# Performance work log

Measured on AMD Instinct MI355X. Metric: run time of the kernel, lower is better.

## Reference

```python
import jax, jax.numpy as jnp
import numpy as np

EPS = 1e-5
NEG_SLOPE = 0.2  # DGL GATConv default leaky_relu slope


def conv1d_same(x, w, b):
    # x: [N, Cin, T], w: [Cout, Cin, K]
    y = jax.lax.conv_general_dilated(x, w, (1,), 'SAME',
                                     dimension_numbers=('NCW', 'OIW', 'NCW'))
    return y + b[None, :, None]


def gated_conv(x, w1, b1, w2, b2, w3, b3):
    # Temporal_Gated_Conv: relu(conv1(x)*sigmoid(conv2(x)) + conv3(x))
    return jax.nn.relu(conv1d_same(x, w1, b1) * jax.nn.sigmoid(conv1d_same(x, w2, b2))
                       + conv1d_same(x, w3, b3))


def bn3(x, g, b):
    # BatchNorm1d on [N, C, T]: stats over (N, T), training mode (batch stats)
    m = jnp.mean(x, (0, 2), keepdims=True)
    v = jnp.var(x, (0, 2), keepdims=True)
    return (x - m) * jax.lax.rsqrt(v + EPS) * g[None, :, None] + b[None, :, None]


def bn2(x, g, b):
    # BatchNorm1d on [N, F]: stats over N
    m = jnp.mean(x, 0, keepdims=True)
    v = jnp.var(x, 0, keepdims=True)
    return (x - m) * jax.lax.rsqrt(v + EPS) * g[None, :] + b[None, :]


def setup_inputs() -> dict:
    key = jax.random.key(0)
    ks = jax.random.split(key, 24)
    N, C, T, H, DEG = 20000, 32, 8, 4, 16
    F = C * T          # GAT in/out feats per head = 256
    E = N * DEG
    s = 0.05
    inp = {
        'X': jax.random.normal(ks[0], (N, C, T), jnp.float32),
        'src': jax.random.randint(ks[1], (E,), 0, N, jnp.int32),
        'dst': jax.random.randint(ks[2], (E,), 0, N, jnp.int32),
        # residual_proj: Conv1d(C->C, k=1)
        'rp_w': jax.random.normal(ks[3], (C, C, 1), jnp.float32) * s,
        'rp_b': jnp.zeros((C,), jnp.float32),
        # gated_conv1: three Conv1d(C->C, k=3)
        'g1_w1': jax.random.normal(ks[4], (C, C, 3), jnp.float32) * s,
        'g1_b1': jnp.zeros((C,), jnp.float32),
        'g1_w2': jax.random.normal(ks[5], (C, C, 3), jnp.float32) * s,
        'g1_b2': jnp.zeros((C,), jnp.float32),
        'g1_w3': jax.random.normal(ks[6], (C, C, 3), jnp.float32) * s,
        'g1_b3': jnp.zeros((C,), jnp.float32),
        'bn0_g': jnp.ones((C,), jnp.float32),
        'bn0_b': jnp.zeros((C,), jnp.float32),
        # GATConv: fc [H*F, F], attn_l/attn_r [H, F], bias [H*F]
        'gat_w': jax.random.normal(ks[7], (H * F, F), jnp.float32) * s,
        'attn_l': jax.random.normal(ks[8], (H, F), jnp.float32) * s,
        'attn_r': jax.random.normal(ks[9], (H, F), jnp.float32) * s,
        'gat_bias': jnp.zeros((H * F,), jnp.float32),
        'bn1_g': jnp.ones((H * F,), jnp.float32),
        'bn1_b': jnp.zeros((H * F,), jnp.float32),
        # gated_conv2: three Conv1d(C*H -> C, k=3)
        'g2_w1': jax.random.normal(ks[10], (C, C * H, 3), jnp.float32) * s,
        'g2_b1': jnp.zeros((C,), jnp.float32),
        'g2_w2': jax.random.normal(ks[11], (C, C * H, 3), jnp.float32) * s,
        'g2_b2': jnp.zeros((C,), jnp.float32),
        'g2_w3': jax.random.normal(ks[12], (C, C * H, 3), jnp.float32) * s,
        'g2_b3': jnp.zeros((C,), jnp.float32),
        'bn2_g': jnp.ones((C,), jnp.float32),
        'bn2_b': jnp.zeros((C,), jnp.float32),
    }
    return inp


def reference(X, src, dst, rp_w, rp_b, g1_w1, g1_b1, g1_w2, g1_b2, g1_w3, g1_b3,
              bn0_g, bn0_b, gat_w, attn_l, attn_r, gat_bias, bn1_g, bn1_b,
              g2_w1, g2_b1, g2_w2, g2_b2, g2_w3, g2_b3, bn2_g, bn2_b):
    N, C, T = X.shape
    H, F = attn_l.shape

    residual = conv1d_same(X, rp_w, rp_b)                      # [N, C, T]
    x = gated_conv(X, g1_w1, g1_b1, g1_w2, g1_b2, g1_w3, g1_b3)
    x = bn3(x, bn0_g, bn0_b)
    x = x.reshape(N, C * T)                                    # row-major flatten == torch .view

    # --- DGL GATConv (feat_drop=attn_drop=0, concat heads, ReLU activation) ---
    h = (x @ gat_w.T).reshape(N, H, F)                         # fc projection
    el = jnp.sum(h * attn_l, -1)                               # [N, H]
    er = jnp.sum(h * attn_r, -1)                               # [N, H]
    e = jax.nn.leaky_relu(el[src] + er[dst], NEG_SLOPE)        # [E, H]
    # segment softmax over incoming edges of each dst node
    m = jax.ops.segment_max(e, dst, num_segments=N)            # [N, H]
    ee = jnp.exp(e - m[dst])
    den = jax.ops.segment_sum(ee, dst, num_segments=N)         # [N, H]
    alpha = ee / den[dst]                                      # [E, H]
    rst = jax.ops.segment_sum(alpha[:, :, None] * h[src], dst, num_segments=N)  # [N, H, F]
    rst = jax.nn.relu(rst + gat_bias.reshape(H, F))

    x = rst.reshape(N, H * F)                                  # concat heads
    x = bn2(x, bn1_g, bn1_b)
    x = x.reshape(N, (H * F) // T, T)                          # [N, C*H, T]
    x = gated_conv(x, g2_w1, g2_b1, g2_w2, g2_b2, g2_w3, g2_b3)
    x = bn3(x, bn2_g, bn2_b)
    x = jax.nn.relu(x + residual)                              # self.last=True, dropout=0
    return x
```

## Files before the change

kernel.cpp:

```cpp
#include <hip/hip_runtime.h>
#include <stdint.h>

#define NN 20000
#define NE 320000

typedef unsigned short us16;
typedef __attribute__((ext_vector_type(8))) short short8;
typedef __attribute__((ext_vector_type(4))) float f32x4;

union U4 { uint4 v; us16 s[8]; unsigned u[4]; };
union U2 { uint2 v; us16 s[4]; };

__device__ __forceinline__ float b2f(us16 u){ return __uint_as_float(((unsigned)u)<<16); }
__device__ __forceinline__ us16 f2b(float f){
  unsigned u = __float_as_uint(f);
  u += 0x7fffu + ((u>>16)&1u);
  return (us16)(u>>16);
}

__global__ __launch_bounds__(256) void k_misc(
    const float* __restrict__ gatw, us16* __restrict__ Wb,
    const float* __restrict__ w1, const float* __restrict__ w2, const float* __restrict__ w3,
    us16* __restrict__ Wt,
    const float* __restrict__ c1w1, const float* __restrict__ c1w2, const float* __restrict__ c1w3,
    const float* __restrict__ rp_w, us16* __restrict__ Wt1,
    const float* __restrict__ attnl, const float* __restrict__ attnr,
    float* __restrict__ wl, float* __restrict__ wr,
    const int* __restrict__ dst, int* __restrict__ counts)
{
  const int b = blockIdx.x, tid = threadIdx.x;
  if(b < 256){
    int i = b*256 + tid;
    float4 v = *(const float4*)(gatw + (size_t)i*4);
    U2 o;
    o.s[0]=f2b(v.x); o.s[1]=f2b(v.y); o.s[2]=f2b(v.z); o.s[3]=f2b(v.w);
    *(uint2*)(Wb + (size_t)i*4) = o.v;
  } else if(b < 400){
    int i = (b-256)*256 + tid;
    int s = i/12288, rem = i%12288;
    int co3 = rem>>7, ci = rem&127;
    const float* w = (co3<32) ? w1 : (co3<64) ? w2 : w3;
    Wt[i] = f2b(w[(co3&31)*384 + ci*3 + s]);
  } else if(b < 448){
    int i = (b-400)*256 + tid;
    int s = i>>12, rem = i&4095;
    int co3 = rem>>5, ci = rem&31;
    float v;
    if(co3 < 96){
      const float* w = (co3<32) ? c1w1 : (co3<64) ? c1w2 : c1w3;
      v = w[(co3&31)*96 + ci*3 + s];
    } else {
      v = (s==1) ? rp_w[(co3-96)*32 + ci] : 0.f;
    }
    Wt1[i] = f2b(v);
  } else if(b < 480){
    int bb = b-448;
    int sel = bb>>4, hd = (bb>>2)&3, fq = bb&3;
    const float* attn = sel ? attnr : attnl;
    int k = tid;
    float s = 0.f;
    int f0 = fq*64;
    #pragma unroll 8
    for(int f=f0; f<f0+64; f++)
      s = fmaf(attn[hd*256+f], gatw[(size_t)(hd*256+f)*256 + k], s);
    atomicAdd(&((sel ? wr : wl)[hd*256+k]), s);
  } else {
    int e = (b-480)*256 + tid;
    if(e < NE) atomicAdd(&counts[dst[e]], 1);
  }
}

__global__ __launch_bounds__(256) void k_gemm1(
    const float* __restrict__ X, const us16* __restrict__ Wt1,
    const float* __restrict__ b1, const float* __restrict__ b2, const float* __restrict__ b3,
    const float* __restrict__ rp_b,
    us16* __restrict__ gc1, us16* __restrict__ resid,
    float* __restrict__ bn0_sum, float* __restrict__ bn0_sq)
{
  __shared__ float smemF[16896];
  us16* As = (us16*)smemF;
  us16* Bs = As + 6400;
  float* Cs = smemF;
  __shared__ float redS[32], redQ[32];
  const int tid = threadIdx.x;
  if(tid<32){ redS[tid]=0.f; redQ[tid]=0.f; }
  const int node0 = blockIdx.x*16;
  const int lane = tid&63, wv = tid>>6;
  const int wm = wv&1, wn = wv>>1;
  const int mrow = lane&15, kg = (lane>>4)*8;
  for(int idx=tid; idx<1024; idx+=256){
    int n = idx>>6, rem = idx&63, slot = (rem>>5)*9, ci = rem&31;
    As[n*400 + slot*40 + ci] = 0;
  }
  #pragma unroll
  for(int i=0;i<4;i++){
    int idx = i*256 + tid;
    int n = idx>>6, rem = idx&63, ci = rem>>1, tq = rem&1;
    float4 xv = *(const float4*)(X + (size_t)(node0+n)*256 + ci*8 + tq*4);
    us16* p = &As[n*400 + (tq*4+1)*40 + ci];
    p[0]   = f2b(xv.x);
    p[40]  = f2b(xv.y);
    p[80]  = f2b(xv.z);
    p[120] = f2b(xv.w);
  }
  #pragma unroll
  for(int i=0;i<6;i++){
    int c = i*256 + tid;
    int s = c>>9, rem = c&511, co = rem>>2, cq = rem&3;
    *(uint4*)&Bs[s*5120 + co*40 + cq*8] = *(const uint4*)(Wt1 + s*4096 + co*32 + cq*8);
  }
  __syncthreads();
  f32x4 acc[4][4] = {};
  #pragma unroll
  for(int s=0; s<3; s++){
    short8 af[4], bfr[4];
    #pragma unroll
    for(int i=0;i<4;i++){
      int r = wm*64 + i*16 + mrow;
      af[i] = *(const short8*)&As[(r>>3)*400 + ((r&7)+s)*40 + kg];
    }
    #pragma unroll
    for(int j=0;j<4;j++)
      bfr[j] = *(const short8*)&Bs[s*5120 + (wn*64 + j*16 + mrow)*40 + kg];
    #pragma unroll
    for(int i=0;i<4;i++){
      #pragma unroll
      for(int j=0;j<4;j++)
        acc[i][j] = __builtin_amdgcn_mfma_f32_16x16x32_bf16(af[i], bfr[j], acc[i][j], 0, 0, 0);
    }
  }
  __syncthreads();
  #pragma unroll
  for(int i=0;i<4;i++){
    #pragma unroll
    for(int j=0;j<4;j++){
      #pragma unroll
      for(int r=0;r<4;r++)
        Cs[(wm*64 + i*16 + (lane>>4)*4 + r)*132 + wn*64 + j*16 + (lane&15)] = acc[i][j][r];
    }
  }
  __syncthreads();
  const int co = tid&31, rg = tid>>5;
  const float bb1=b1[co], bb2=b2[co], bb3=b3[co], bbr=rp_b[co];
  float s=0.f, q=0.f;
  #pragma unroll
  for(int half=0; half<2; half++){
    U4 ov, rv;
    #pragma unroll
    for(int t=0;t<8;t++){
      int r = rg*16 + half*8 + t;
      float c1 = Cs[r*132 + co]      + bb1;
      float c2 = Cs[r*132 + co + 32] + bb2;
      float c3 = Cs[r*132 + co + 64] + bb3;
      float rr = Cs[r*132 + co + 96] + bbr;
      float sg = 1.f/(1.f+__expf(-c2));
      float v = fmaf(c1, sg, c3);
      v = v>0.f ? v : 0.f;
      s += v; q += v*v;
      ov.s[t] = f2b(v);
      rv.s[t] = f2b(rr);
    }
    int node = node0 + rg*2 + half;
    *(uint4*)(gc1   + (size_t)node*256 + co*8) = ov.v;
    *(uint4*)(resid + (size_t)node*256 + co*8) = rv.v;
  }
  atomicAdd(&redS[co], s); atomicAdd(&redQ[co], q);
  __syncthreads();
  if(tid<32)      atomicAdd(&bn0_sum[tid], redS[tid]);
  else if(tid<64) atomicAdd(&bn0_sq[tid-32], redQ[tid-32]);
}

__global__ __launch_bounds__(256) void k_eler2(const us16* __restrict__ gc1,
    const float* __restrict__ bn0_sum, const float* __restrict__ bn0_sq,
    const float* __restrict__ bn0g, const float* __restrict__ bn0b,
    const float* __restrict__ wl, const float* __restrict__ wr,
    float* __restrict__ el, float* __restrict__ er,
    const int* __restrict__ counts, int* __restrict__ offsets, int* __restrict__ cursor)
{
  const int tid = threadIdx.x;
  if(blockIdx.x < 5000){
    __shared__ float sa[32], sb[32];
    if(tid<32){
      float m = bn0_sum[tid]*(1.f/160000.f);
      float v = bn0_sq[tid]*(1.f/160000.f) - m*m;
      float a = bn0g[tid]*rsqrtf(v + 1e-5f);
      sa[tid] = a; sb[tid] = bn0b[tid] - m*a;
    }
    __syncthreads();
    const int wv = tid>>6, lane = tid&63;
    const int node = blockIdx.x*4 + wv;
    U2 g; g.v = *(const uint2*)(gc1 + (size_t)node*256 + lane*4);
    const float a = sa[lane>>1], b = sb[lane>>1];
    float xv[4];
    #pragma unroll
    for(int j=0;j<4;j++) xv[j] = fmaf(a, b2f(g.s[j]), b);
    float res[8];
    #pragma unroll
    for(int hd=0; hd<4; hd++){
      float4 lv = *(const float4*)(wl + hd*256 + lane*4);
      float4 rv = *(const float4*)(wr + hd*256 + lane*4);
      res[hd]   = xv[0]*lv.x + xv[1]*lv.y + xv[2]*lv.z + xv[3]*lv.w;
      res[4+hd] = xv[0]*rv.x + xv[1]*rv.y + xv[2]*rv.z + xv[3]*rv.w;
    }
    #pragma unroll
    for(int o=32;o;o>>=1){
      #pragma unroll
      for(int k=0;k<8;k++) res[k] += __shfl_xor(res[k], o, 64);
    }
    if(lane==0){
      #pragma unroll
      for(int hd=0;hd<4;hd++){ el[node*4+hd]=res[hd]; er[node*4+hd]=res[4+hd]; }
    }
  } else {
    __shared__ int buf[256];
    const int base = tid*79;
    int s = 0;
    for(int j=0;j<79;j++){
      int idx = base+j;
      if(idx<NN) s += counts[idx];
    }
    buf[tid] = s;
    __syncthreads();
    for(int off=1; off<256; off<<=1){
      int t = (tid>=off) ? buf[tid-off] : 0;
      __syncthreads();
      buf[tid] += t;
      __syncthreads();
    }
    int excl = buf[tid] - s;
    for(int j=0;j<79;j++){
      int idx = base+j;
      if(idx<NN){
        offsets[idx]=excl; cursor[idx]=excl;
        excl += counts[idx];
      }
    }
    if(tid==255) offsets[NN] = buf[255];
  }
}

__global__ __launch_bounds__(256) void k_scatter(const int* __restrict__ src, const int* __restrict__ dst,
    int* __restrict__ cursor, int* __restrict__ esrc,
    const float* __restrict__ el, const float* __restrict__ er,
    float* __restrict__ ew)
{
  int e = blockIdx.x*256 + threadIdx.x;
  if(e < NE){
    int s = src[e], d = dst[e];
    int pos = atomicAdd(&cursor[d], 1);
    esrc[pos] = s;
    float4 lv = *(const float4*)(el + s*4);
    float4 rv = *(const float4*)(er + d*4);
    float4 sc;
    sc.x = lv.x+rv.x; sc.x = sc.x>0.f ? sc.x : 0.2f*sc.x;
    sc.y = lv.y+rv.y; sc.y = sc.y>0.f ? sc.y : 0.2f*sc.y;
    sc.z = lv.z+rv.z; sc.z = sc.z>0.f ? sc.z : 0.2f*sc.z;
    sc.w = lv.w+rv.w; sc.w = sc.w>0.f ? sc.w : 0.2f*sc.w;
    *(float4*)(ew + (size_t)pos*4) = sc;
  }
}

__global__ __launch_bounds__(256) void k_agg2(
    const int* __restrict__ offsets, const int* __restrict__ esrc,
    const float* __restrict__ ew, const us16* __restrict__ gc1,
    const float* __restrict__ bn0_sum, const float* __restrict__ bn0_sq,
    const float* __restrict__ bn0g, const float* __restrict__ bn0b,
    us16* __restrict__ Axg)
{
  const int tid = threadIdx.x;
  const int wv = tid>>6, lane = tid&63;
  const int node = blockIdx.x*4 + wv;
  const int ch = lane>>1;
  float mmn = bn0_sum[ch]*(1.f/160000.f);
  float vvn = bn0_sq[ch]*(1.f/160000.f) - mmn*mmn;
  float sa = bn0g[ch]*rsqrtf(vvn + 1e-5f);
  float sb = bn0b[ch] - mmn*sa;
  const int beg = offsets[node];
  const int deg = offsets[node+1] - beg;
  const int h = lane>>4, i0 = lane&15;
  float m = -3.0e38f;
  for(int i=i0; i<deg; i+=16) m = fmaxf(m, ew[(size_t)(beg+i)*4 + h]);
  m = fmaxf(m, __shfl_xor(m,1,64)); m = fmaxf(m, __shfl_xor(m,2,64));
  m = fmaxf(m, __shfl_xor(m,4,64)); m = fmaxf(m, __shfl_xor(m,8,64));
  float den = 0.f;
  for(int i=i0; i<deg; i+=16) den += __expf(ew[(size_t)(beg+i)*4 + h] - m);
  den += __shfl_xor(den,1,64); den += __shfl_xor(den,2,64);
  den += __shfl_xor(den,4,64); den += __shfl_xor(den,8,64);
  const float m0=__shfl(m,0,64),   m1=__shfl(m,16,64),  m2=__shfl(m,32,64),  m3=__shfl(m,48,64);
  const float d0=__shfl(den,0,64), d1=__shfl(den,16,64),d2=__shfl(den,32,64),d3=__shfl(den,48,64);
  const float v0=d0>0.f?1.f/d0:0.f, v1=d1>0.f?1.f/d1:0.f,
              v2=d2>0.f?1.f/d2:0.f, v3=d3>0.f?1.f/d3:0.f;
  float a0c[4]={},a1c[4]={},a2c[4]={},a3c[4]={};
  #pragma unroll 4
  for(int j=0; j<deg; j++){
    int pos = beg+j;
    float4 w4 = *(const float4*)(ew + (size_t)pos*4);
    int sN = esrc[pos];
    U2 hv; hv.v = *(const uint2*)(gc1 + (size_t)sN*256 + lane*4);
    float e0 = __expf(w4.x-m0)*v0;
    float e1 = __expf(w4.y-m1)*v1;
    float e2 = __expf(w4.z-m2)*v2;
    float e3 = __expf(w4.w-m3)*v3;
    #pragma unroll
    for(int kk=0;kk<4;kk++){
      float x = b2f(hv.s[kk]);
      a0c[kk] = fmaf(e0,x,a0c[kk]);
      a1c[kk] = fmaf(e1,x,a1c[kk]);
      a2c[kk] = fmaf(e2,x,a2c[kk]);
      a3c[kk] = fmaf(e3,x,a3c[kk]);
    }
  }
  const float sbi = sb * ((deg>0)?1.f:0.f);
  U2 o0,o1,o2,o3;
  #pragma unroll
  for(int kk=0;kk<4;kk++){
    o0.s[kk]=f2b(fmaf(sa,a0c[kk],sbi));
    o1.s[kk]=f2b(fmaf(sa,a1c[kk],sbi));
    o2.s[kk]=f2b(fmaf(sa,a2c[kk],sbi));
    o3.s[kk]=f2b(fmaf(sa,a3c[kk],sbi));
  }
  *(uint2*)(Axg + ((size_t)node)*256            + lane*4) = o0.v;
  *(uint2*)(Axg + ((size_t)NN + node)*256       + lane*4) = o1.v;
  *(uint2*)(Axg + ((size_t)2*NN + node)*256     + lane*4) = o2.v;
  *(uint2*)(Axg + ((size_t)3*NN + node)*256     + lane*4) = o3.v;
}

__global__ __launch_bounds__(256) void k_gemm3(const us16* __restrict__ Axg, const us16* __restrict__ Wb,
    const float* __restrict__ gbias, us16* __restrict__ rst,
    float* __restrict__ bn1_sum, float* __restrict__ bn1_sq)
{
  __shared__ us16 As[128*40];
  __shared__ us16 Bs[128*40];
  const int tid = threadIdx.x;
  const int row0 = blockIdx.x*128;
  const int cb   = blockIdx.y*128;
  const int hd   = blockIdx.z;
  const us16* A = Axg + (size_t)hd*NN*256;
  const us16* B = Wb  + (size_t)(hd*256 + cb)*256;
  const int lane = tid&63, wv = tid>>6;
  const int wm = wv&1, wn = wv>>1;
  const int mrow = lane&15, kg = (lane>>4)*8;
  f32x4 acc[4][4] = {};
  for(int k0=0; k0<256; k0+=32){
    #pragma unroll
    for(int i=0;i<2;i++){
      int chunk = i*256 + tid;
      int row = chunk>>2, cc = chunk&3;
      int g = row0 + row;
      uint4 av; av.x=0;av.y=0;av.z=0;av.w=0;
      if(g < NN) av = *(const uint4*)(A + (size_t)g*256 + k0 + cc*8);
      *(uint4*)&As[row*40 + cc*8] = av;
      *(uint4*)&Bs[row*40 + cc*8] = *(const uint4*)(B + (size_t)row*256 + k0 + cc*8);
    }
    __syncthreads();
    short8 af[4], bfr[4];
    #pragma unroll
    for(int i=0;i<4;i++) af[i]  = *(const short8*)&As[(wm*64 + i*16 + mrow)*40 + kg];
    #pragma unroll
    for(int j=0;j<4;j++) bfr[j] = *(const short8*)&Bs[(wn*64 + j*16 + mrow)*40 + kg];
    #pragma unroll
    for(int i=0;i<4;i++){
      #pragma unroll
      for(int j=0;j<4;j++)
        acc[i][j] = __builtin_amdgcn_mfma_f32_16x16x32_bf16(af[i], bfr[j], acc[i][j], 0, 0, 0);
    }
    __syncthreads();
  }
  float gb[4];
  #pragma unroll
  for(int j=0;j<4;j++)
    gb[j] = gbias[hd*256 + cb + wn*64 + j*16 + (lane&15)];
  float cs[4]={}, cq[4]={};
  #pragma unroll
  for(int i=0;i<4;i++){
    #pragma unroll
    for(int j=0;j<4;j++){
      #pragma unroll
      for(int r=0;r<4;r++){
        int g = row0 + wm*64 + i*16 + (lane>>4)*4 + r;
        if(g < NN){
          float v = acc[i][j][r] + gb[j];
          v = v>0.f ? v : 0.f;
          rst[(size_t)g*1024 + hd*256 + cb + wn*64 + j*16 + (lane&15)] = f2b(v);
          cs[j] += v; cq[j] += v*v;
        }
      }
    }
  }
  #pragma unroll
  for(int j=0;j<4;j++){
    cs[j] += __shfl_xor(cs[j],16,64); cs[j] += __shfl_xor(cs[j],32,64);
    cq[j] += __shfl_xor(cq[j],16,64); cq[j] += __shfl_xor(cq[j],32,64);
  }
  if(lane < 16){
    #pragma unroll
    for(int j=0;j<4;j++){
      int col = hd*256 + cb + wn*64 + j*16 + lane;
      atomicAdd(&bn1_sum[col], cs[j]);
      atomicAdd(&bn1_sq[col],  cq[j]);
    }
  }
}

__global__ __launch_bounds__(256) void k_gemm2(
    const us16* __restrict__ rst, const us16* __restrict__ Wt,
    const float* __restrict__ bn1_sum, const float* __restrict__ bn1_sq,
    const float* __restrict__ bn1g, const float* __restrict__ bn1b,
    const float* __restrict__ b1, const float* __restrict__ b2, const float* __restrict__ b3,
    us16* __restrict__ y2, float* __restrict__ bn2_sum, float* __restrict__ bn2_sq)
{
  __shared__ float smemF[16384];
  float* s1a = smemF;
  float* s1b = smemF + 1024;
  us16* As = (us16*)(smemF + 2048);
  us16* Bs = As + 21760;
  float* Cs = (float*)(smemF + 2048);
  __shared__ float redS[32], redQ[32];
  const int tid = threadIdx.x;
  if(tid<32){ redS[tid]=0.f; redQ[tid]=0.f; }
  const int node0 = blockIdx.x*16;
  const int lane = tid&63, wv = tid>>6;
  const int wm = wv&1, wn = wv>>1;
  const int mrow = lane&15, kg = (lane>>4)*8;
  for(int f=tid; f<1024; f+=256){
    float m = bn1_sum[f]*(1.f/20000.f);
    float v = bn1_sq[f]*(1.f/20000.f) - m*m;
    float a = bn1g[f]*rsqrtf(v + 1e-5f);
    int l = (f&7)*128 + (f>>3);
    s1a[l] = a; s1b[l] = bn1b[f] - m*a;
  }
  for(int idx=tid; idx<4096; idx+=256){
    int n = idx>>8, rem = idx&255, slot = (rem>>7)*9, ci = rem&127;
    As[n*1360 + slot*136 + ci] = 0;
  }
  __syncthreads();
  #pragma unroll
  for(int i=0;i<8;i++){
    int idx = i*256 + tid;
    int n = idx>>7, ci = idx&127;
    U4 in; in.v = *(const uint4*)(rst + (size_t)(node0+n)*1024 + ci*8);
    us16* p = &As[n*1360 + 136 + ci];
    #pragma unroll
    for(int t=0;t<8;t++){
      float a = s1a[t*128+ci], b = s1b[t*128+ci];
      p[t*136] = f2b(fmaf(a, b2f(in.s[t]), b));
    }
  }
  f32x4 acc[4][3] = {};
  for(int rd=0; rd<6; rd++){
    const int s = rd>>1, kc = rd&1;
    __syncthreads();
    #pragma unroll
    for(int i=0;i<3;i++){
      int chunk = i*256 + tid;
      int brow = chunk>>3, cc = chunk&7;
      *(uint4*)&Bs[brow*72 + cc*8] =
        *(const uint4*)(Wt + s*12288 + brow*128 + kc*64 + cc*8);
    }
    __syncthreads();
    #pragma unroll
    for(int kk=0; kk<64; kk+=32){
      short8 af[4], bfr[3];
      #pragma unroll
      for(int i=0;i<4;i++){
        int r = wm*64 + i*16 + mrow;
        af[i] = *(const short8*)&As[(r>>3)*1360 + ((r&7)+s)*136 + kc*64 + kk + kg];
      }
      #pragma unroll
      for(int j=0;j<3;j++)
        bfr[j] = *(const short8*)&Bs[(wn*48 + j*16 + mrow)*72 + kk + kg];
      #pragma unroll
      for(int i=0;i<4;i++){
        #pragma unroll
        for(int j=0;j<3;j++)
          acc[i][j] = __builtin_amdgcn_mfma_f32_16x16x32_bf16(af[i], bfr[j], acc[i][j], 0, 0, 0);
      }
    }
  }
  __syncthreads();
  #pragma unroll
  for(int i=0;i<4;i++){
    #pragma unroll
    for(int j=0;j<3;j++){
      #pragma unroll
      for(int r=0;r<4;r++)
        Cs[(wm*64 + i*16 + (lane>>4)*4 + r)*100 + wn*48 + j*16 + (lane&15)] = acc[i][j][r];
    }
  }
  __syncthreads();
  const int co = tid&31, rg = tid>>5;
  const float bb1=b1[co], bb2=b2[co], bb3=b3[co];
  float s=0.f, q=0.f;
  #pragma unroll
  for(int half=0; half<2; half++){
    U4 ov;
    #pragma unroll
    for(int t=0;t<8;t++){
      int r = rg*16 + half*8 + t;
      float c1 = Cs[r*100 + co]      + bb1;
      float c2 = Cs[r*100 + co + 32] + bb2;
      float c3 = Cs[r*100 + co + 64] + bb3;
      float sg = 1.f/(1.f+__expf(-c2));
      float v = fmaf(c1, sg, c3);
      v = v>0.f ? v : 0.f;
      s += v; q += v*v;
      ov.s[t] = f2b(v);
    }
    int node = node0 + rg*2 + half;
    *(uint4*)(y2 + (size_t)node*256 + co*8) = ov.v;
  }
  atomicAdd(&redS[co], s); atomicAdd(&redQ[co], q);
  __syncthreads();
  if(tid<32)      atomicAdd(&bn2_sum[tid], redS[tid]);
  else if(tid<64) atomicAdd(&bn2_sq[tid-32], redQ[tid-32]);
}

__global__ __launch_bounds__(256) void k_final(const us16* __restrict__ y2,
    const float* __restrict__ bn2_sum, const float* __restrict__ bn2_sq,
    const float* __restrict__ bn2g, const float* __restrict__ bn2b,
    const us16* __restrict__ resid, float* __restrict__ out)
{
  __shared__ float fa[32], fb[32];
  const int tid = threadIdx.x;
  if(tid<32){
    float m = bn2_sum[tid]*(1.f/160000.f);
    float v = bn2_sq[tid]*(1.f/160000.f) - m*m;
    float a = bn2g[tid]*rsqrtf(v + 1e-5f);
    fa[tid] = a; fb[tid] = bn2b[tid] - m*a;
  }
  __syncthreads();
  size_t base = ((size_t)blockIdx.x*256 + tid)*8;
  int ch = (int)((base>>3)&31);
  float a = fa[ch], b = fb[ch];
  U4 yv, rv;
  yv.v = *(const uint4*)(y2+base);
  rv.v = *(const uint4*)(resid+base);
  float4 o0, o1;
  float vv[8];
  #pragma unroll
  for(int j=0;j<8;j++){
    float v = fmaf(a, b2f(yv.s[j]), b) + b2f(rv.s[j]);
    vv[j] = v>0.f ? v : 0.f;
  }
  o0.x=vv[0]; o0.y=vv[1]; o0.z=vv[2]; o0.w=vv[3];
  o1.x=vv[4]; o1.y=vv[5]; o1.z=vv[6]; o1.w=vv[7];
  *(float4*)(out+base)   = o0;
  *(float4*)(out+base+4) = o1;
}

extern "C" void kernel_launch(void* const* d_in, const int* in_sizes, int n_in,
                              void* d_out, int out_size, void* d_ws, size_t ws_size,
                              hipStream_t stream)
{
  const float* X    = (const float*)d_in[0];
  const int*  src   = (const int*)d_in[1];
  const int*  dst   = (const int*)d_in[2];
  const float* rp_w = (const float*)d_in[3];
  const float* rp_b = (const float*)d_in[4];
  const float* g1w1 = (const float*)d_in[5];
  const float* g1b1 = (const float*)d_in[6];
  const float* g1w2 = (const float*)d_in[7];
  const float* g1b2 = (const float*)d_in[8];
  const float* g1w3 = (const float*)d_in[9];
  const float* g1b3 = (const float*)d_in[10];
  const float* bn0g = (const float*)d_in[11];
  const float* bn0b = (const float*)d_in[12];
  const float* gatw = (const float*)d_in[13];
  const float* attnl= (const float*)d_in[14];
  const float* attnr= (const float*)d_in[15];
  const float* gbias= (const float*)d_in[16];
  const float* bn1g = (const float*)d_in[17];
  const float* bn1b = (const float*)d_in[18];
  const float* g2w1 = (const float*)d_in[19];
  const float* g2b1 = (const float*)d_in[20];
  const float* g2w2 = (const float*)d_in[21];
  const float* g2b2 = (const float*)d_in[22];
  const float* g2w3 = (const float*)d_in[23];
  const float* g2b3 = (const float*)d_in[24];
  const float* bn2g = (const float*)d_in[25];
  const float* bn2b = (const float*)d_in[26];
  float* out = (float*)d_out;
  (void)in_sizes; (void)n_in; (void)out_size; (void)ws_size;

  char* w = (char*)d_ws;
  float* bn0_sum = (float*)w;
  float* bn0_sq  = bn0_sum + 32;
  float* bn1_sum = bn0_sum + 64;
  float* bn1_sq  = bn1_sum + 1024;
  float* bn2_sum = bn1_sq  + 1024;
  float* bn2_sq  = bn2_sum + 32;
  float* wl      = bn2_sq + 32;
  float* wr      = wl + 1024;
  int*   counts  = (int*)(wr + 1024);
  size_t zeroBytes = (size_t)((char*)(counts + NN) - w);
  int*   offsets = counts + NN;
  int*   cursor  = offsets + 20004;
  int*   esrc    = cursor + NN;
  float* el      = (float*)(esrc + NE);
  float* er      = el + NN*4;
  float* ew      = er + NN*4;
  us16*  wb      = (us16*)(ew + (size_t)NE*4);
  us16*  resid   = wb + 262144;
  us16*  gc1     = resid + 5120000;
  us16*  Axg     = gc1   + 5120000;
  us16*  rst     = Axg   + 20480000;
  us16*  Wt      = rst   + 20480000;
  us16*  Wt1     = Wt    + 36864;
  us16*  y2      = gc1;

  hipMemsetAsync(d_ws, 0, zeroBytes, stream);
  k_misc<<<1730, 256, 0, stream>>>(gatw, wb, g2w1, g2w2, g2w3, Wt,
                                   g1w1, g1w2, g1w3, rp_w, Wt1,
                                   attnl, attnr, wl, wr, dst, counts);
  k_gemm1<<<1250, 256, 0, stream>>>(X, Wt1, g1b1, g1b2, g1b3, rp_b,
                                    gc1, resid, bn0_sum, bn0_sq);
  k_eler2<<<5001, 256, 0, stream>>>(gc1, bn0_sum, bn0_sq, bn0g, bn0b, wl, wr, el, er,
                                    counts, offsets, cursor);
  k_scatter<<<1250, 256, 0, stream>>>(src, dst, cursor, esrc, el, er, ew);
  k_agg2<<<5000, 256, 0, stream>>>(offsets, esrc, ew, gc1, bn0_sum, bn0_sq, bn0g, bn0b, Axg);
  k_gemm3<<<dim3(157, 2, 4), 256, 0, stream>>>(Axg, wb, gbias, rst, bn1_sum, bn1_sq);
  k_gemm2<<<1250, 256, 0, stream>>>(rst, Wt, bn1_sum, bn1_sq, bn1g, bn1b,
                                    g2b1, g2b2, g2b3, y2, bn2_sum, bn2_sq);
  k_final<<<2500, 256, 0, stream>>>(y2, bn2_sum, bn2_sq, bn2g, bn2b, resid, out);
}
```

Before: 401.9 us.

## Move CSR prefix scan into gemm1 and halve gemm2 shared-memory footprint

The single-block prefix scan over per-node in-degree counts moves from the element-wise el/er kernel into an extra block of the first GEMM kernel. That block stages the counts in shared memory as 16-bit values before scanning, so the serial tail overlaps with the GEMM instead of delaying the next kernel. The second gated-conv GEMM now loads and normalises its A tile in two K halves rather than all at once, cutting shared memory from 64KB to 50KB to allow more resident blocks. The cost is extra barriers and repeated B-tile loads per K half, and the 16-bit count storage assumes no node has more than 65535 incoming edges.

```diff
diff --git a/kernel.cpp b/kernel.cpp
--- a/kernel.cpp
+++ b/kernel.cpp
@@ -75,167 +75,170 @@
     const float* __restrict__ b1, const float* __restrict__ b2, const float* __restrict__ b3,
     const float* __restrict__ rp_b,
     us16* __restrict__ gc1, us16* __restrict__ resid,
-    float* __restrict__ bn0_sum, float* __restrict__ bn0_sq)
+    float* __restrict__ bn0_sum, float* __restrict__ bn0_sq,
+    const int* __restrict__ counts, int* __restrict__ offsets, int* __restrict__ cursor)
 {
   __shared__ float smemF[16896];
-  us16* As = (us16*)smemF;
-  us16* Bs = As + 6400;
-  float* Cs = smemF;
   __shared__ float redS[32], redQ[32];
   const int tid = threadIdx.x;
-  if(tid<32){ redS[tid]=0.f; redQ[tid]=0.f; }
-  const int node0 = blockIdx.x*16;
-  const int lane = tid&63, wv = tid>>6;
-  const int wm = wv&1, wn = wv>>1;
-  const int mrow = lane&15, kg = (lane>>4)*8;
-  for(int idx=tid; idx<1024; idx+=256){
-    int n = idx>>6, rem = idx&63, slot = (rem>>5)*9, ci = rem&31;
-    As[n*400 + slot*40 + ci] = 0;
-  }
-  #pragma unroll
-  for(int i=0;i<4;i++){
-    int idx = i*256 + tid;
-    int n = idx>>6, rem = idx&63, ci = rem>>1, tq = rem&1;
-    float4 xv = *(const float4*)(X + (size_t)(node0+n)*256 + ci*8 + tq*4);
-    us16* p = &As[n*400 + (tq*4+1)*40 + ci];
-    p[0]   = f2b(xv.x);
-    p[40]  = f2b(xv.y);
-    p[80]  = f2b(xv.z);
-    p[120] = f2b(xv.w);
-  }
-  #pragma unroll
-  for(int i=0;i<6;i++){
-    int c = i*256 + tid;
-    int s = c>>9, rem = c&511, co = rem>>2, cq = rem&3;
-    *(uint4*)&Bs[s*5120 + co*40 + cq*8] = *(const uint4*)(Wt1 + s*4096 + co*32 + cq*8);
-  }
-  __syncthreads();
-  f32x4 acc[4][4] = {};
-  #pragma unroll
-  for(int s=0; s<3; s++){
-    short8 af[4], bfr[4];
+  if(blockIdx.x < 1250){
+    us16* As = (us16*)smemF;
+    us16* Bs = As + 6400;
+    float* Cs = smemF;
+    if(tid<32){ redS[tid]=0.f; redQ[tid]=0.f; }
+    const int node0 = blockIdx.x*16;
+    const int lane = tid&63, wv = tid>>6;
+    const int wm = wv&1, wn = wv>>1;
+    const int mrow = lane&15, kg = (lane>>4)*8;
+    for(int idx=tid; idx<1024; idx+=256){
+      int n = idx>>6, rem = idx&63, slot = (rem>>5)*9, ci = rem&31;
+      As[n*400 + slot*40 + ci] = 0;
+    }
     #pragma unroll
     for(int i=0;i<4;i++){
-      int r = wm*64 + i*16 + mrow;
-      af[i] = *(const short8*)&As[(r>>3)*400 + ((r&7)+s)*40 + kg];
-    }
-    #pragma unroll
-    for(int j=0;j<4;j++)
-      bfr[j] = *(const short8*)&Bs[s*5120 + (wn*64 + j*16 + mrow)*40 + kg];
+      int idx = i*256 + tid;
+      int n = idx>>6, rem = idx&63, ci = rem>>1, tq = rem&1;
+      float4 xv = *(const float4*)(X + (size_t)(node0+n)*256 + ci*8 + tq*4);
+      us16* p = &As[n*400 + (tq*4+1)*40 + ci];
+      p[0]   = f2b(xv.x);
+      p[40]  = f2b(xv.y);
+      p[80]  = f2b(xv.z);
+      p[120] = f2b(xv.w);
+    }
+    #pragma unroll
+    for(int i=0;i<6;i++){
+      int c = i*256 + tid;
+      int s = c>>9, rem = c&511, co = rem>>2, cq = rem&3;
+      *(uint4*)&Bs[s*5120 + co*40 + cq*8] = *(const uint4*)(Wt1 + s*4096 + co*32 + cq*8);
+    }
+    __syncthreads();
+    f32x4 acc[4][4] = {};
+    #pragma unroll
+    for(int s=0; s<3; s++){
+      short8 af[4], bfr[4];
+      #pragma unroll
+      for(int i=0;i<4;i++){
+        int r = wm*64 + i*16 + mrow;
+        af[i] = *(const short8*)&As[(r>>3)*400 + ((r&7)+s)*40 + kg];
+      }
+      #pragma unroll
+      for(int j=0;j<4;j++)
+        bfr[j] = *(const short8*)&Bs[s*5120 + (wn*64 + j*16 + mrow)*40 + kg];
+      #pragma unroll
+      for(int i=0;i<4;i++){
+        #pragma unroll
+        for(int j=0;j<4;j++)
+          acc[i][j] = __builtin_amdgcn_mfma_f32_16x16x32_bf16(af[i], bfr[j], acc[i][j], 0, 0, 0);
+      }
+    }
+    __syncthreads();
     #pragma unroll
     for(int i=0;i<4;i++){
       #pragma unroll
-      for(int j=0;j<4;j++)
-        acc[i][j] = __builtin_amdgcn_mfma_f32_16x16x32_bf16(af[i], bfr[j], acc[i][j], 0, 0, 0);
-    }
-  }
-  __syncthreads();
-  #pragma unroll
-  for(int i=0;i<4;i++){
-    #pragma unroll
-    for(int j=0;j<4;j++){
-      #pragma unroll
-      for(int r=0;r<4;r++)
-        Cs[(wm*64 + i*16 + (lane>>4)*4 + r)*132 + wn*64 + j*16 + (lane&15)] = acc[i][j][r];
-    }
-  }
-  __syncthreads();
-  const int co = tid&31, rg = tid>>5;
-  const float bb1=b1[co], bb2=b2[co], bb3=b3[co], bbr=rp_b[co];
-  float s=0.f, q=0.f;
-  #pragma unroll
-  for(int half=0; half<2; half++){
-    U4 ov, rv;
-    #pragma unroll
-    for(int t=0;t<8;t++){
-      int r = rg*16 + half*8 + t;
-      float c1 = Cs[r*132 + co]      + bb1;
-      float c2 = Cs[r*132 + co + 32] + bb2;
-      float c3 = Cs[r*132 + co + 64] + bb3;
-      float rr = Cs[r*132 + co + 96] + bbr;
-      float sg = 1.f/(1.f+__expf(-c2));
-      float v = fmaf(c1, sg, c3);
-      v = v>0.f ? v : 0.f;
-      s += v; q += v*v;
-      ov.s[t] = f2b(v);
-      rv.s[t] = f2b(rr);
-    }
-    int node = node0 + rg*2 + half;
-    *(uint4*)(gc1   + (size_t)node*256 + co*8) = ov.v;
-    *(uint4*)(resid + (size_t)node*256 + co*8) = rv.v;
-  }
-  atomicAdd(&redS[co], s); atomicAdd(&redQ[co], q);
-  __syncthreads();
-  if(tid<32)      atomicAdd(&bn0_sum[tid], redS[tid]);
-  else if(tid<64) atomicAdd(&bn0_sq[tid-32], redQ[tid-32]);
+      for(int j=0;j<4;j++){
+        #pragma unroll
+        for(int r=0;r<4;r++)
+          Cs[(wm*64 + i*16 + (lane>>4)*4 + r)*132 + wn*64 + j*16 + (lane&15)] = acc[i][j][r];
+      }
+    }
+    __syncthreads();
+    const int co = tid&31, rg = tid>>5;
+    const float bb1=b1[co], bb2=b2[co], bb3=b3[co], bbr=rp_b[co];
+    float s=0.f, q=0.f;
+    #pragma unroll
+    for(int half=0; half<2; half++){
+      U4 ov, rv;
+      #pragma unroll
+      for(int t=0;t<8;t++){
+        int r = rg*16 + half*8 + t;
+        float c1 = Cs[r*132 + co]      + bb1;
+        float c2 = Cs[r*132 + co + 32] + bb2;
+        float c3 = Cs[r*132 + co + 64] + bb3;
+        float rr = Cs[r*132 + co + 96] + bbr;
+        float sg = 1.f/(1.f+__expf(-c2));
+        float v = fmaf(c1, sg, c3);
+        v = v>0.f ? v : 0.f;
+        s += v; q += v*v;
+        ov.s[t] = f2b(v);
+        rv.s[t] = f2b(rr);
+      }
+      int node = node0 + rg*2 + half;
+      *(uint4*)(gc1   + (size_t)node*256 + co*8) = ov.v;
+      *(uint4*)(resid + (size_t)node*256 + co*8) = rv.v;
+    }
+    atomicAdd(&redS[co], s); atomicAdd(&redQ[co], q);
+    __syncthreads();
+    if(tid<32)      atomicAdd(&bn0_sum[tid], redS[tid]);
+    else if(tid<64) atomicAdd(&bn0_sq[tid-32], redQ[tid-32]);
+  } else {
+    us16* cnt  = (us16*)smemF;
+    int*  wsum = (int*)(smemF + 12800);
+    for(int r=0;r<79;r++){
+      int idx = r*256 + tid;
+      cnt[idx] = (idx<NN) ? (us16)counts[idx] : (us16)0;
+    }
+    __syncthreads();
+    const int base = tid*79;
+    int s = 0;
+    for(int j=0;j<79;j++) s += cnt[base+j];
+    wsum[tid] = s;
+    __syncthreads();
+    for(int off=1; off<256; off<<=1){
+      int t = (tid>=off) ? wsum[tid-off] : 0;
+      __syncthreads();
+      wsum[tid] += t;
+      __syncthreads();
+    }
+    int excl = wsum[tid] - s;
+    for(int j=0;j<79;j++){
+      int idx = base+j;
+      if(idx<NN){
+        offsets[idx]=excl; cursor[idx]=excl;
+        excl += cnt[idx];
+      }
+    }
+    if(tid==255) offsets[NN] = wsum[255];
+  }
 }
 
 __global__ __launch_bounds__(256) void k_eler2(const us16* __restrict__ gc1,
     const float* __restrict__ bn0_sum, const float* __restrict__ bn0_sq,
     const float* __restrict__ bn0g, const float* __restrict__ bn0b,
     const float* __restrict__ wl, const float* __restrict__ wr,
-    float* __restrict__ el, float* __restrict__ er,
-    const int* __restrict__ counts, int* __restrict__ offsets, int* __restrict__ cursor)
-{
+    float* __restrict__ el, float* __restrict__ er)
+{
+  __shared__ float sa[32], sb[32];
   const int tid = threadIdx.x;
-  if(blockIdx.x < 5000){
-    __shared__ float sa[32], sb[32];
-    if(tid<32){
-      float m = bn0_sum[tid]*(1.f/160000.f);
-      float v = bn0_sq[tid]*(1.f/160000.f) - m*m;
-      float a = bn0g[tid]*rsqrtf(v + 1e-5f);
-      sa[tid] = a; sb[tid] = bn0b[tid] - m*a;
-    }
-    __syncthreads();
-    const int wv = tid>>6, lane = tid&63;
-    const int node = blockIdx.x*4 + wv;
-    U2 g; g.v = *(const uint2*)(gc1 + (size_t)node*256 + lane*4);
-    const float a = sa[lane>>1], b = sb[lane>>1];
-    float xv[4];
-    #pragma unroll
-    for(int j=0;j<4;j++) xv[j] = fmaf(a, b2f(g.s[j]), b);
-    float res[8];
-    #pragma unroll
-    for(int hd=0; hd<4; hd++){
-      float4 lv = *(const float4*)(wl + hd*256 + lane*4);
-      float4 rv = *(const float4*)(wr + hd*256 + lane*4);
-      res[hd]   = xv[0]*lv.x + xv[1]*lv.y + xv[2]*lv.z + xv[3]*lv.w;
-      res[4+hd] = xv[0]*rv.x + xv[1]*rv.y + xv[2]*rv.z + xv[3]*rv.w;
-    }
-    #pragma unroll
-    for(int o=32;o;o>>=1){
-      #pragma unroll
-      for(int k=0;k<8;k++) res[k] += __shfl_xor(res[k], o, 64);
-    }
-    if(lane==0){
-      #pragma unroll
-      for(int hd=0;hd<4;hd++){ el[node*4+hd]=res[hd]; er[node*4+hd]=res[4+hd]; }
-    }
-  } else {
-    __shared__ int buf[256];
-    const int base = tid*79;
-    int s = 0;
-    for(int j=0;j<79;j++){
-      int idx = base+j;
-      if(idx<NN) s += counts[idx];
-    }
-    buf[tid] = s;
-    __syncthreads();
-    for(int off=1; off<256; off<<=1){
-      int t = (tid>=off) ? buf[tid-off] : 0;
-      __syncthreads();
-      buf[tid] += t;
-      __syncthreads();
-    }
-    int excl = buf[tid] - s;
-    for(int j=0;j<79;j++){
-      int idx = base+j;
-      if(idx<NN){
-        offsets[idx]=excl; cursor[idx]=excl;
-        excl += counts[idx];
-      }
-    }
-    if(tid==255) offsets[NN] = buf[255];
+  if(tid<32){
+    float m = bn0_sum[tid]*(1.f/160000.f);
+    float v = bn0_sq[tid]*(1.f/160000.f) - m*m;
+    float a = bn0g[tid]*rsqrtf(v + 1e-5f);
+    sa[tid] = a; sb[tid] = bn0b[tid] - m*a;
+  }
+  __syncthreads();
+  const int wv = tid>>6, lane = tid&63;
+  const int node = blockIdx.x*4 + wv;
+  U2 g; g.v = *(const uint2*)(gc1 + (size_t)node*256 + lane*4);
+  const float a = sa[lane>>1], b = sb[lane>>1];
+  float xv[4];
+  #pragma unroll
+  for(int j=0;j<4;j++) xv[j] = fmaf(a, b2f(g.s[j]), b);
+  float res[8];
+  #pragma unroll
+  for(int hd=0; hd<4; hd++){
+    float4 lv = *(const float4*)(wl + hd*256 + lane*4);
+    float4 rv = *(const float4*)(wr + hd*256 + lane*4);
+    res[hd]   = xv[0]*lv.x + xv[1]*lv.y + xv[2]*lv.z + xv[3]*lv.w;
+    res[4+hd] = xv[0]*rv.x + xv[1]*rv.y + xv[2]*rv.z + xv[3]*rv.w;
+  }
+  #pragma unroll
+  for(int o=32;o;o>>=1){
+    #pragma unroll
+    for(int k=0;k<8;k++) res[k] += __shfl_xor(res[k], o, 64);
+  }
+  if(lane==0){
+    #pragma unroll
+    for(int hd=0;hd<4;hd++){ el[node*4+hd]=res[hd]; er[node*4+hd]=res[4+hd]; }
   }
 }
 
@@ -409,12 +412,12 @@
     const float* __restrict__ b1, const float* __restrict__ b2, const float* __restrict__ b3,
     us16* __restrict__ y2, float* __restrict__ bn2_sum, float* __restrict__ bn2_sq)
 {
-  __shared__ float smemF[16384];
+  __shared__ float smemF[12800];
   float* s1a = smemF;
   float* s1b = smemF + 1024;
   us16* As = (us16*)(smemF + 2048);
-  us16* Bs = As + 21760;
-  float* Cs = (float*)(smemF + 2048);
+  us16* Bs = As + 11520;
+  float* Cs = smemF;
   __shared__ float redS[32], redQ[32];
   const int tid = threadIdx.x;
   if(tid<32){ redS[tid]=0.f; redQ[tid]=0.f; }
@@ -429,51 +432,54 @@
     int l = (f&7)*128 + (f>>3);
     s1a[l] = a; s1b[l] = bn1b[f] - m*a;
   }
-  for(int idx=tid; idx<4096; idx+=256){
-    int n = idx>>8, rem = idx&255, slot = (rem>>7)*9, ci = rem&127;
-    As[n*1360 + slot*136 + ci] = 0;
+  for(int idx=tid; idx<2048; idx+=256){
+    int n = idx>>7, rem = idx&127, slot = (rem>>6)*9, ci = rem&63;
+    As[n*720 + slot*72 + ci] = 0;
   }
   __syncthreads();
-  #pragma unroll
-  for(int i=0;i<8;i++){
-    int idx = i*256 + tid;
-    int n = idx>>7, ci = idx&127;
-    U4 in; in.v = *(const uint4*)(rst + (size_t)(node0+n)*1024 + ci*8);
-    us16* p = &As[n*1360 + 136 + ci];
-    #pragma unroll
-    for(int t=0;t<8;t++){
-      float a = s1a[t*128+ci], b = s1b[t*128+ci];
-      p[t*136] = f2b(fmaf(a, b2f(in.s[t]), b));
-    }
-  }
   f32x4 acc[4][3] = {};
-  for(int rd=0; rd<6; rd++){
-    const int s = rd>>1, kc = rd&1;
-    __syncthreads();
-    #pragma unroll
-    for(int i=0;i<3;i++){
-      int chunk = i*256 + tid;
-      int brow = chunk>>3, cc = chunk&7;
-      *(uint4*)&Bs[brow*72 + cc*8] =
-        *(const uint4*)(Wt + s*12288 + brow*128 + kc*64 + cc*8);
-    }
-    __syncthreads();
-    #pragma unroll
-    for(int kk=0; kk<64; kk+=32){
-      short8 af[4], bfr[3];
-      #pragma unroll
-      for(int i=0;i<4;i++){
-        int r = wm*64 + i*16 + mrow;
-        af[i] = *(const short8*)&As[(r>>3)*1360 + ((r&7)+s)*136 + kc*64 + kk + kg];
-      }
-      #pragma unroll
-      for(int j=0;j<3;j++)
-        bfr[j] = *(const short8*)&Bs[(wn*48 + j*16 + mrow)*72 + kk + kg];
-      #pragma unroll
-      for(int i=0;i<4;i++){
+  for(int kc=0; kc<2; kc++){
+    if(kc) __syncthreads();
+    #pragma unroll
+    for(int i=0;i<4;i++){
+      int idx = i*256 + tid;
+      int n = idx>>6, cil = idx&63;
+      int ci = kc*64 + cil;
+      U4 in; in.v = *(const uint4*)(rst + (size_t)(node0+n)*1024 + ci*8);
+      us16* p = &As[n*720 + 72 + cil];
+      #pragma unroll
+      for(int t=0;t<8;t++){
+        float a = s1a[t*128+ci], b = s1b[t*128+ci];
+        p[t*72] = f2b(fmaf(a, b2f(in.s[t]), b));
+      }
+    }
+    for(int s=0; s<3; s++){
+      if(s) __syncthreads();
+      #pragma unroll
+      for(int i=0;i<3;i++){
+        int chunk = i*256 + tid;
+        int brow = chunk>>3, cc = chunk&7;
+        *(uint4*)&Bs[brow*72 + cc*8] =
+          *(const uint4*)(Wt + s*12288 + brow*128 + kc*64 + cc*8);
+      }
+      __syncthreads();
+      #pragma unroll
+      for(int kk=0; kk<64; kk+=32){
+        short8 af[4], bfr[3];
+        #pragma unroll
+        for(int i=0;i<4;i++){
+          int r = wm*64 + i*16 + mrow;
+          af[i] = *(const short8*)&As[(r>>3)*720 + ((r&7)+s)*72 + kk + kg];
+        }
         #pragma unroll
         for(int j=0;j<3;j++)
-          acc[i][j] = __builtin_amdgcn_mfma_f32_16x16x32_bf16(af[i], bfr[j], acc[i][j], 0, 0, 0);
+          bfr[j] = *(const short8*)&Bs[(wn*48 + j*16 + mrow)*72 + kk + kg];
+        #pragma unroll
+        for(int i=0;i<4;i++){
+          #pragma unroll
+          for(int j=0;j<3;j++)
+            acc[i][j] = __builtin_amdgcn_mfma_f32_16x16x32_bf16(af[i], bfr[j], acc[i][j], 0, 0, 0);
+        }
       }
     }
   }
@@ -612,10 +618,10 @@
   k_misc<<<1730, 256, 0, stream>>>(gatw, wb, g2w1, g2w2, g2w3, Wt,
                                    g1w1, g1w2, g1w3, rp_w, Wt1,
                                    attnl, attnr, wl, wr, dst, counts);
-  k_gemm1<<<1250, 256, 0, stream>>>(X, Wt1, g1b1, g1b2, g1b3, rp_b,
-                                    gc1, resid, bn0_sum, bn0_sq);
-  k_eler2<<<5001, 256, 0, stream>>>(gc1, bn0_sum, bn0_sq, bn0g, bn0b, wl, wr, el, er,
+  k_gemm1<<<1251, 256, 0, stream>>>(X, Wt1, g1b1, g1b2, g1b3, rp_b,
+                                    gc1, resid, bn0_sum, bn0_sq,
                                     counts, offsets, cursor);
+  k_eler2<<<5000, 256, 0, stream>>>(gc1, bn0_sum, bn0_sq, bn0g, bn0b, wl, wr, el, er);
   k_scatter<<<1250, 256, 0, stream>>>(src, dst, cursor, esrc, el, er, ew);
   k_agg2<<<5000, 256, 0, stream>>>(offsets, esrc, ew, gc1, bn0_sum, bn0_sq, bn0g, bn0b, Axg);
   k_gemm3<<<dim3(157, 2, 4), 256, 0, stream>>>(Axg, wb, gbias, rst, bn1_sum, bn1_sq);
```

Measured after the change: 381.6 us. 5.0% less time.
